# Kernel optimization log

Measured on AMD Instinct MI355X. Metric: run time of the kernel, lower is better.

## Reference

```python
import jax, jax.numpy as jnp
import numpy as np
from jax.scipy.linalg import expm

N_T = 320    # time grid points
N_S = 16     # state dim n
P_IN = 8     # input dim p
M_OUT = 8    # output dim m
LT = 0.1     # SE length scale
TMAX = 1.0   # time horizon
EPS = 1e-3

_expm_b = jax.vmap(expm)

def _build_A(V1_raw, V2_raw, V3_raw):
    # parametrizations: L_plus, L, Skew (from torch module)
    n = V1_raw.shape[0]
    eye = jnp.eye(n, dtype=V1_raw.dtype)
    V1 = jnp.tril(V1_raw, -1) + jnp.diag(jnp.abs(jnp.diag(V1_raw))) + EPS * eye
    V2 = jnp.tril(V2_raw)
    V3u = jnp.triu(V3_raw, 1)
    V3 = V3u - V3u.T
    # get_AP: P_inv = V1^{-T} V1^{-1}; A = -0.5 P_inv V2 V2^T + P_inv V3
    V1_inv = jnp.linalg.inv(V1 + EPS * eye)
    P_inv = V1_inv.T @ V1_inv
    A = -0.5 * (P_inv @ (V2 @ V2.T)) + P_inv @ V3
    return A

def _forward(V1_raw, V2_raw, V3_raw, B_w, C_w, D_w, mean_x0, covar_x0, mean_U, mean_dU):
    A = _build_A(V1_raw, V2_raw, V3_raw)
    N = mean_U.shape[0]
    n = A.shape[0]
    T = jnp.linspace(0.0, TMAX, N)            # dT == integration grid (k_i = i)
    step = T[1] - T[0]

    # --- mean_module term1: C expm(A t_i) mean_x0 ---
    E_t = _expm_b(A[None, :, :] * T[:, None, None])          # (N, n, n)
    term1 = jnp.einsum('mn,inj,j->im', C_w, E_t, mean_x0)     # (N, m)

    # --- Greens1 on the full (t_i - t_j) grid, masked to j <= i ---
    idx = jnp.arange(N)
    lower = (idx[None, :] <= idx[:, None])                    # j <= i
    dt_full = T[:, None] - T[None, :]                         # (N, N)
    dt = jnp.where(lower, dt_full, 0.0)                       # expm(0)=I where unused
    Epair = _expm_b((A[None, :, :] * dt.reshape(-1)[:, None, None])).reshape(N, N, n, n)
    G1 = jnp.einsum('mn,ijnk,kp->ijmp', C_w, Epair, B_w)      # (N, N, m, p)

    # trapezoid weights over j in [0, i]: step*[0.5,1,...,1,0.5]; zero row for i=0
    w = jnp.where(lower,
                  jnp.where((idx[None, :] == 0) | (idx[None, :] == idx[:, None]), 0.5, 1.0),
                  0.0) * step
    w = w * (idx[:, None] > 0)
    term2 = jnp.einsum('ijmp,jp,ij->im', G1, mean_U, w)       # (N, m)

    # --- term3: D u_d(t_i) ---
    term3 = mean_dU @ D_w.T                                   # (N, m)
    mean_y = term1 + term2 + term3

    # --- covar_module term1: C expm(A t_i) covar_x0 expm(A t_j)^T C^T ---
    CE = jnp.einsum('mn,ink->imk', C_w, E_t)                  # (N, m, n)
    covar1 = jnp.einsum('imk,kl,jol->ijmo', CE, covar_x0, CE) # (N, N, m, m)

    # --- SE kernel over the integration grid ---
    covar_U = jnp.exp(-0.5 * (dt_full ** 2) / (LT * LT))      # (N, N)
    return mean_y, covar1, covar_U

def setup_inputs() -> dict:
    key = jax.random.key(0)
    ks = jax.random.split(key, 10)
    n, p, m, N = N_S, P_IN, M_OUT, N_T
    V1_raw = jnp.eye(n) + 0.1 * jax.random.normal(ks[0], (n, n), jnp.float32)
    V2_raw = 0.1 * jax.random.normal(ks[1], (n, n), jnp.float32)
    V3_raw = 0.1 * jax.random.normal(ks[2], (n, n), jnp.float32)
    B_w = 0.1 * jax.random.normal(ks[3], (n, p), jnp.float32)
    C_w = 0.1 * jax.random.normal(ks[4], (m, n), jnp.float32)
    D_w = 0.1 * jax.random.normal(ks[5], (m, p), jnp.float32)
    mean_x0 = jax.random.normal(ks[6], (n,), jnp.float32)
    S = jax.random.normal(ks[7], (n, n), jnp.float32)
    covar_x0 = S @ S.T / n + 0.1 * jnp.eye(n)   # PSD initial covariance
    mean_U = jax.random.normal(ks[8], (N, p), jnp.float32)
    mean_dU = jax.random.normal(ks[9], (N, p), jnp.float32)
    return {"V1_raw": V1_raw, "V2_raw": V2_raw, "V3_raw": V3_raw,
            "B_w": B_w, "C_w": C_w, "D_w": D_w,
            "mean_x0": mean_x0, "covar_x0": covar_x0,
            "mean_U": mean_U, "mean_dU": mean_dU}

def reference(V1_raw, V2_raw, V3_raw, B_w, C_w, D_w, mean_x0, covar_x0, mean_U, mean_dU):
    return _forward(V1_raw, V2_raw, V3_raw, B_w, C_w, D_w,
                    mean_x0, covar_x0, mean_U, mean_dU)
```

## Files before the change

### kernel.cpp

```cpp
#include <hip/hip_runtime.h>
#include <math.h>

#define NT 320
#define NS 16
#define PIN 8
#define MOUT 8
#define STEPF (1.0f/319.0f)


__device__ __forceinline__ float4 wave_mm(const float4 A, const float4 B,
                                          const int lane) {
    float4 c = make_float4(0.f, 0.f, 0.f, 0.f);
    const int rowbase = lane & 60;
    const int jb = lane & 3;
#pragma unroll
    for (int k = 0; k < 16; ++k) {
        const int srcA = rowbase | (k >> 2);
        float a;
        if ((k & 3) == 0)      a = __shfl(A.x, srcA);
        else if ((k & 3) == 1) a = __shfl(A.y, srcA);
        else if ((k & 3) == 2) a = __shfl(A.z, srcA);
        else                   a = __shfl(A.w, srcA);
        const int srcB = (k << 2) | jb;
        c.x += a * __shfl(B.x, srcB);
        c.y += a * __shfl(B.y, srcB);
        c.z += a * __shfl(B.z, srcB);
        c.w += a * __shfl(B.w, srcB);
    }
    return c;
}

__device__ __forceinline__ float4 wave_mm_abt(const float4 A, const float4 B,
                                              const int lane) {
    float4 c = make_float4(0.f, 0.f, 0.f, 0.f);
    const int rowbase = lane & 60;
    const int jb = lane & 3;
#pragma unroll
    for (int k = 0; k < 16; ++k) {
        const int hk = k >> 2;
        float a, b0, b1, b2, b3;
        if ((k & 3) == 0) {
            a  = __shfl(A.x, rowbase | hk);
            b0 = __shfl(B.x, (jb << 4) | 0 | hk);
            b1 = __shfl(B.x, (jb << 4) | 4 | hk);
            b2 = __shfl(B.x, (jb << 4) | 8 | hk);
            b3 = __shfl(B.x, (jb << 4) | 12 | hk);
        } else if ((k & 3) == 1) {
            a  = __shfl(A.y, rowbase | hk);
            b0 = __shfl(B.y, (jb << 4) | 0 | hk);
            b1 = __shfl(B.y, (jb << 4) | 4 | hk);
            b2 = __shfl(B.y, (jb << 4) | 8 | hk);
            b3 = __shfl(B.y, (jb << 4) | 12 | hk);
        } else if ((k & 3) == 2) {
            a  = __shfl(A.z, rowbase | hk);
            b0 = __shfl(B.z, (jb << 4) | 0 | hk);
            b1 = __shfl(B.z, (jb << 4) | 4 | hk);
            b2 = __shfl(B.z, (jb << 4) | 8 | hk);
            b3 = __shfl(B.z, (jb << 4) | 12 | hk);
        } else {
            a  = __shfl(A.w, rowbase | hk);
            b0 = __shfl(B.w, (jb << 4) | 0 | hk);
            b1 = __shfl(B.w, (jb << 4) | 4 | hk);
            b2 = __shfl(B.w, (jb << 4) | 8 | hk);
            b3 = __shfl(B.w, (jb << 4) | 12 | hk);
        }
        c.x += a * b0; c.y += a * b1; c.z += a * b2; c.w += a * b3;
    }
    return c;
}

__global__ __launch_bounds__(64) void k_phase1(
        const float* __restrict__ V1r,
        const float* __restrict__ V2r,
        const float* __restrict__ V3r,
        const float* __restrict__ C_w,
        const float* __restrict__ B_w,
        const float* __restrict__ cov0,
        const float* __restrict__ x0,
        float* __restrict__ CE_g,
        float* __restrict__ Mrow_g,
        float* __restrict__ G_g,
        float* __restrict__ y1_g) {
    __shared__ float Msub[16][16];
    __shared__ float MinvT[16][16];
    __shared__ float V3s[16][16];
    const int lane = threadIdx.x;
    const int row = lane >> 2, jb = lane & 3;
    const int k = blockIdx.x;
    const float t = (float)k * STEPF;

    const float4 v1 = *((const float4*)(V1r + row * 16 + jb * 4));
    const float4 v2 = *((const float4*)(V2r + row * 16 + jb * 4));
    const float4 v3raw = *((const float4*)(V3r + row * 16 + jb * 4));

    float4 Mf, V2f;
    {
        const float mv[4] = {v1.x, v1.y, v1.z, v1.w};
        const float vv[4] = {v2.x, v2.y, v2.z, v2.w};
        float mo[4], vo[4];
#pragma unroll
        for (int m = 0; m < 4; ++m) {
            const int col = jb * 4 + m;
            mo[m] = (row > col) ? mv[m]
                  : ((row == col) ? (fabsf(mv[m]) + 2.0f * 1e-3f) : 0.0f);
            vo[m] = (col <= row) ? vv[m] : 0.0f;
        }
        Mf  = make_float4(mo[0], mo[1], mo[2], mo[3]);
        V2f = make_float4(vo[0], vo[1], vo[2], vo[3]);
    }
    *((float4*)&Msub[row][jb * 4]) = Mf;
    *((float4*)&V3s[row][jb * 4])  = v3raw;
    __syncthreads();

    if (lane < 16) {
        const int c = lane;
        float x[16];
#pragma unroll
        for (int r = 0; r < 16; ++r) {
            float s = (r == c) ? 1.0f : 0.0f;
#pragma unroll
            for (int kk = 0; kk < 16; ++kk) {
                if (kk < r) s -= Msub[r][kk] * x[kk];
            }
            x[r] = (r < c) ? 0.0f : s / Msub[r][r];
        }
#pragma unroll
        for (int r = 0; r < 16; ++r) MinvT[c][r] = x[r];
    }
    __syncthreads();

    float4 V3f;
    {
        float o[4];
#pragma unroll
        for (int m = 0; m < 4; ++m) {
            const int col = jb * 4 + m;
            const float up = V3s[row][col];
            const float lo = V3s[col][row];
            o[m] = (col > row) ? up : ((row > col) ? -lo : 0.0f);
        }
        V3f = make_float4(o[0], o[1], o[2], o[3]);
    }
    const float4 Tf = *((const float4*)&MinvT[row][jb * 4]);

    const float4 Pinvf = wave_mm_abt(Tf, Tf, lane);
    float4 Wf = wave_mm_abt(V2f, V2f, lane);
    Wf.x = -0.5f * Wf.x + V3f.x;
    Wf.y = -0.5f * Wf.y + V3f.y;
    Wf.z = -0.5f * Wf.z + V3f.z;
    Wf.w = -0.5f * Wf.w + V3f.w;
    const float4 Af = wave_mm(Pinvf, Wf, lane);

    float s0 = fabsf(Af.x) + fabsf(Af.y) + fabsf(Af.z) + fabsf(Af.w);
    s0 += __shfl_xor(s0, 1);
    s0 += __shfl_xor(s0, 2);
    float nrm = s0;
    nrm = fmaxf(nrm, __shfl_xor(nrm, 4));
    nrm = fmaxf(nrm, __shfl_xor(nrm, 8));
    nrm = fmaxf(nrm, __shfl_xor(nrm, 16));
    nrm = fmaxf(nrm, __shfl_xor(nrm, 32));

    float nt = nrm * t;
    int s = 0;
    while (nt > 0.5f && s < 30) { nt *= 0.5f; ++s; }
    const float scale = t * exp2f((float)(-s));
    float4 Bh;
    Bh.x = Af.x * scale; Bh.y = Af.y * scale;
    Bh.z = Af.z * scale; Bh.w = Af.w * scale;

    float4 idf;
    idf.x = (row == 4 * jb + 0) ? 1.0f : 0.0f;
    idf.y = (row == 4 * jb + 1) ? 1.0f : 0.0f;
    idf.z = (row == 4 * jb + 2) ? 1.0f : 0.0f;
    idf.w = (row == 4 * jb + 3) ? 1.0f : 0.0f;

    float4 P;
    P.x = idf.x + Bh.x * (1.0f / 9.0f);
    P.y = idf.y + Bh.y * (1.0f / 9.0f);
    P.z = idf.z + Bh.z * (1.0f / 9.0f);
    P.w = idf.w + Bh.w * (1.0f / 9.0f);
#pragma unroll
    for (int d = 8; d >= 1; --d) {
        const float4 c = wave_mm(Bh, P, lane);
        const float inv = 1.0f / (float)d;
        P.x = idf.x + c.x * inv;
        P.y = idf.y + c.y * inv;
        P.z = idf.z + c.z * inv;
        P.w = idf.w + c.w * inv;
    }
    for (int q = 0; q < s; ++q) P = wave_mm(P, P, lane);

    const int crow = row & 7;
    const float4 Cf  = *((const float4*)(C_w + crow * 16 + jb * 4));
    const float4 CEf = wave_mm(Cf, P, lane);
    const float4 covf = *((const float4*)(cov0 + row * 16 + jb * 4));
    const float4 Mrowf = wave_mm(CEf, covf, lane);
    float4 Bwf = make_float4(0.f, 0.f, 0.f, 0.f);
    if (jb < 2) Bwf = *((const float4*)(B_w + row * 8 + jb * 4));
    const float4 Gf = wave_mm(CEf, Bwf, lane);
    const float4 x0f = *((const float4*)(x0 + jb * 4));
    float yp = CEf.x * x0f.x + CEf.y * x0f.y + CEf.z * x0f.z + CEf.w * x0f.w;
    yp += __shfl_xor(yp, 1);
    yp += __shfl_xor(yp, 2);

    if (row < 8) {
        *((float4*)(CE_g   + k * 128 + row * 16 + jb * 4)) = CEf;
        *((float4*)(Mrow_g + k * 128 + row * 16 + jb * 4)) = Mrowf;
        if (jb < 2) *((float4*)(G_g + k * 64 + row * 8 + jb * 4)) = Gf;
        if (jb == 0) y1_g[k * 8 + row] = yp;
    }
}

__global__ void k_phase2(const float* __restrict__ Mrow_g,
                         const float* __restrict__ CE_g,
                         const float* __restrict__ y1_g,
                         const float* __restrict__ G_g,
                         const float* __restrict__ U,
                         const float* __restrict__ dU,
                         const float* __restrict__ D_w,
                         float* __restrict__ out_c1,
                         float* __restrict__ out_cu,
                         float* __restrict__ out_mean) {
    const int bx  = blockIdx.x;
    const int i   = blockIdx.y;
    const int tid = threadIdx.x;

    if (bx < 20) {
        __shared__ float Mi[128];
        __shared__ float CEj[2048];
        const int jg = bx;
        {
            const float4* srcC = (const float4*)(CE_g + jg * 2048);
            float4* dstC = (float4*)CEj;
            dstC[tid]       = srcC[tid];
            dstC[tid + 256] = srcC[tid + 256];
            if (tid < 32) ((float4*)Mi)[tid] = ((const float4*)(Mrow_g + i * 128))[tid];
        }
        __syncthreads();

        const int jj = tid >> 4;
        const int a  = (tid >> 1) & 7;
        const int bg = tid & 1;
        const float* mi = Mi + a * 16;
        const float* ce = CEj + jj * 128 + bg * 64;
        float r[4];
#pragma unroll
        for (int b = 0; b < 4; ++b) {
            float acc = 0.0f;
#pragma unroll
            for (int l = 0; l < 16; ++l) acc += mi[l] * ce[b * 16 + l];
            r[b] = acc;
        }
        const int j = jg * 16 + jj;
        float4* dst = (float4*)(out_c1 + ((size_t)(i * 320 + j)) * 64 + a * 8 + bg * 4);
        *dst = make_float4(r[0], r[1], r[2], r[3]);

        if (tid < 16) {
            const int jx = jg * 16 + tid;
            const float d = (float)(i - jx) * STEPF;
            out_cu[i * 320 + jx] = expf(-50.0f * d * d);
        }
    } else {
        __shared__ float part[256];
        const int m  = tid & 7;
        const int js = tid >> 3;
        float acc = 0.0f;
        if (i > 0) {
            for (int j = js; j <= i; j += 32) {
                const float w = ((j == 0) || (j == i)) ? 0.5f : 1.0f;
                const float4* Gr = (const float4*)(G_g + (i - j) * 64 + m * 8);
                const float4* Ur = (const float4*)(U + j * 8);
                const float4 g0 = Gr[0], g1 = Gr[1];
                const float4 u0 = Ur[0], u1 = Ur[1];
                float d = g0.x * u0.x + g0.y * u0.y + g0.z * u0.z + g0.w * u0.w
                        + g1.x * u1.x + g1.y * u1.y + g1.z * u1.z + g1.w * u1.w;
                acc += w * d;
            }
        }
        part[tid] = acc;
        __syncthreads();
#pragma unroll
        for (int off = 128; off >= 8; off >>= 1) {
            if (tid < off) part[tid] += part[tid + off];
            __syncthreads();
        }
        if (tid < 8) {
            float t3 = 0.0f;
#pragma unroll
            for (int p = 0; p < 8; ++p) t3 += D_w[tid * 8 + p] * dU[i * 8 + p];
            out_mean[i * 8 + tid] = y1_g[i * 8 + tid] + STEPF * part[tid] + t3;
        }
    }
}

extern "C" void kernel_launch(void* const* d_in, const int* in_sizes, int n_in,
                              void* d_out, int out_size, void* d_ws, size_t ws_size,
                              hipStream_t stream) {
    const float* V1r  = (const float*)d_in[0];
    const float* V2r  = (const float*)d_in[1];
    const float* V3r  = (const float*)d_in[2];
    const float* B_w  = (const float*)d_in[3];
    const float* C_w  = (const float*)d_in[4];
    const float* D_w  = (const float*)d_in[5];
    const float* x0   = (const float*)d_in[6];
    const float* cov0 = (const float*)d_in[7];
    const float* U    = (const float*)d_in[8];
    const float* dU   = (const float*)d_in[9];

    float* ws   = (float*)d_ws;
    float* CE   = ws;
    float* Mrow = CE + 40960;
    float* G    = Mrow + 40960;
    float* y1   = G + 20480;

    float* out      = (float*)d_out;
    float* out_mean = out;
    float* out_c1   = out + 2560;
    float* out_cu   = out + 2560 + 320*320*64;

    k_phase1<<<NT, 64, 0, stream>>>(V1r, V2r, V3r, C_w, B_w, cov0, x0,
                                    CE, Mrow, G, y1);
    k_phase2<<<dim3(21, NT), 256, 0, stream>>>(Mrow, CE, y1, G, U, dU, D_w,
                                               out_c1, out_cu, out_mean);
}
```

Baseline: 106.9 us.

## Restructure covariance outer product: one block per row, transposed CE, LDS-staged stores

Phase 1 now writes CE transposed (channel-major, time-minor) so each phase-2 thread can load its column with coalesced reads. Phase 2 assigns one block of 320 threads per output row i, with each thread computing a full 8x8 tile for one j in registers. It then stages the tiles through padded shared memory in two passes to emit fully coalesced float4 stores of the large output. The mean reduction moves to a separate set of 320 blocks in a 1D grid. This cuts repeated CE staging per block and improves store coalescing, at the cost of 64 accumulators per thread and strided scalar writes in phase 1.

```diff
diff --git a/kernel.cpp b/kernel.cpp
--- a/kernel.cpp
+++ b/kernel.cpp
@@ -77,7 +77,7 @@
         const float* __restrict__ B_w,
         const float* __restrict__ cov0,
         const float* __restrict__ x0,
-        float* __restrict__ CE_g,
+        float* __restrict__ CEt_g,
         float* __restrict__ Mrow_g,
         float* __restrict__ G_g,
         float* __restrict__ y1_g) {
@@ -204,68 +204,91 @@
     yp += __shfl_xor(yp, 2);
 
     if (row < 8) {
-        *((float4*)(CE_g   + k * 128 + row * 16 + jb * 4)) = CEf;
+        const int ch = row * 16 + jb * 4;
+        CEt_g[(ch + 0) * 320 + k] = CEf.x;
+        CEt_g[(ch + 1) * 320 + k] = CEf.y;
+        CEt_g[(ch + 2) * 320 + k] = CEf.z;
+        CEt_g[(ch + 3) * 320 + k] = CEf.w;
         *((float4*)(Mrow_g + k * 128 + row * 16 + jb * 4)) = Mrowf;
         if (jb < 2) *((float4*)(G_g + k * 64 + row * 8 + jb * 4)) = Gf;
         if (jb == 0) y1_g[k * 8 + row] = yp;
     }
 }
 
-__global__ void k_phase2(const float* __restrict__ Mrow_g,
-                         const float* __restrict__ CE_g,
-                         const float* __restrict__ y1_g,
-                         const float* __restrict__ G_g,
-                         const float* __restrict__ U,
-                         const float* __restrict__ dU,
-                         const float* __restrict__ D_w,
-                         float* __restrict__ out_c1,
-                         float* __restrict__ out_cu,
-                         float* __restrict__ out_mean) {
-    const int bx  = blockIdx.x;
-    const int i   = blockIdx.y;
+__global__ __launch_bounds__(320) void k_phase2(
+        const float* __restrict__ Mrow_g,
+        const float* __restrict__ CEt_g,
+        const float* __restrict__ y1_g,
+        const float* __restrict__ G_g,
+        const float* __restrict__ U,
+        const float* __restrict__ dU,
+        const float* __restrict__ D_w,
+        float* __restrict__ out_c1,
+        float* __restrict__ out_cu,
+        float* __restrict__ out_mean) {
+    const int bid = blockIdx.x;
     const int tid = threadIdx.x;
 
-    if (bx < 20) {
-        __shared__ float Mi[128];
-        __shared__ float CEj[2048];
-        const int jg = bx;
+    if (bid < NT) {
+        __shared__ float obuf[160 * 68];
+        const int i = bid;
+        const int j = tid;
+
         {
-            const float4* srcC = (const float4*)(CE_g + jg * 2048);
-            float4* dstC = (float4*)CEj;
-            dstC[tid]       = srcC[tid];
-            dstC[tid + 256] = srcC[tid + 256];
-            if (tid < 32) ((float4*)Mi)[tid] = ((const float4*)(Mrow_g + i * 128))[tid];
-        }
-        __syncthreads();
-
-        const int jj = tid >> 4;
-        const int a  = (tid >> 1) & 7;
-        const int bg = tid & 1;
-        const float* mi = Mi + a * 16;
-        const float* ce = CEj + jj * 128 + bg * 64;
-        float r[4];
-#pragma unroll
-        for (int b = 0; b < 4; ++b) {
-            float acc = 0.0f;
-#pragma unroll
-            for (int l = 0; l < 16; ++l) acc += mi[l] * ce[b * 16 + l];
-            r[b] = acc;
-        }
-        const int j = jg * 16 + jj;
-        float4* dst = (float4*)(out_c1 + ((size_t)(i * 320 + j)) * 64 + a * 8 + bg * 4);
-        *dst = make_float4(r[0], r[1], r[2], r[3]);
-
-        if (tid < 16) {
-            const int jx = jg * 16 + tid;
-            const float d = (float)(i - jx) * STEPF;
-            out_cu[i * 320 + jx] = expf(-50.0f * d * d);
+            const float d = (float)(i - j) * STEPF;
+            out_cu[i * 320 + j] = expf(-50.0f * d * d);
+        }
+
+        const float* __restrict__ mi = Mrow_g + i * 128;
+        const float* __restrict__ ce = CEt_g + j;
+        float acc[8][8];
+#pragma unroll
+        for (int a = 0; a < 8; ++a)
+#pragma unroll
+            for (int b = 0; b < 8; ++b) acc[a][b] = 0.0f;
+
+#pragma unroll
+        for (int l = 0; l < 16; ++l) {
+            float cv[8], mv[8];
+#pragma unroll
+            for (int b = 0; b < 8; ++b) cv[b] = ce[(b * 16 + l) * 320];
+#pragma unroll
+            for (int a = 0; a < 8; ++a) mv[a] = mi[a * 16 + l];
+#pragma unroll
+            for (int a = 0; a < 8; ++a)
+#pragma unroll
+                for (int b = 0; b < 8; ++b) acc[a][b] += mv[a] * cv[b];
+        }
+
+        float4* __restrict__ dst = (float4*)(out_c1 + (size_t)i * 20480);
+#pragma unroll
+        for (int pass = 0; pass < 2; ++pass) {
+            const int jr = j - 160 * pass;
+            if (jr >= 0 && jr < 160) {
+#pragma unroll
+                for (int a = 0; a < 8; ++a) {
+                    *((float4*)&obuf[jr * 68 + a * 8]) =
+                        make_float4(acc[a][0], acc[a][1], acc[a][2], acc[a][3]);
+                    *((float4*)&obuf[jr * 68 + a * 8 + 4]) =
+                        make_float4(acc[a][4], acc[a][5], acc[a][6], acc[a][7]);
+                }
+            }
+            __syncthreads();
+#pragma unroll
+            for (int r = 0; r < 8; ++r) {
+                const int q  = tid + 320 * r;
+                const int jj = q >> 4, cc = q & 15;
+                dst[pass * 2560 + q] = *((const float4*)&obuf[jj * 68 + cc * 4]);
+            }
+            __syncthreads();
         }
     } else {
-        __shared__ float part[256];
+        __shared__ float part[320];
+        const int i  = bid - NT;
         const int m  = tid & 7;
         const int js = tid >> 3;
         float acc = 0.0f;
-        if (i > 0) {
+        if (tid < 256 && i > 0) {
             for (int j = js; j <= i; j += 32) {
                 const float w = ((j == 0) || (j == i)) ? 0.5f : 1.0f;
                 const float4* Gr = (const float4*)(G_g + (i - j) * 64 + m * 8);
@@ -277,7 +300,7 @@
                 acc += w * d;
             }
         }
-        part[tid] = acc;
+        part[tid] = (tid < 256) ? acc : 0.0f;
         __syncthreads();
 #pragma unroll
         for (int off = 128; off >= 8; off >>= 1) {
@@ -308,8 +331,8 @@
     const float* dU   = (const float*)d_in[9];
 
     float* ws   = (float*)d_ws;
-    float* CE   = ws;
-    float* Mrow = CE + 40960;
+    float* CEt  = ws;
+    float* Mrow = CEt + 40960;
     float* G    = Mrow + 40960;
     float* y1   = G + 20480;
 
@@ -319,7 +342,7 @@
     float* out_cu   = out + 2560 + 320*320*64;
 
     k_phase1<<<NT, 64, 0, stream>>>(V1r, V2r, V3r, C_w, B_w, cov0, x0,
-                                    CE, Mrow, G, y1);
-    k_phase2<<<dim3(21, NT), 256, 0, stream>>>(Mrow, CE, y1, G, U, dU, D_w,
-                                               out_c1, out_cu, out_mean);
-}
+                                    CEt, Mrow, G, y1);
+    k_phase2<<<2 * NT, 320, 0, stream>>>(Mrow, CEt, y1, G, U, dU, D_w,
+                                         out_c1, out_cu, out_mean);
+}
```

Measured after the change: 106.8 us. Within noise of the previous version (-0.2%).
